# Kernel optimization log

Hardware: AMD Instinct MI355X
Metric: run time of the kernel (lower is better)

The kernel has to match this reference:

```python
import jax, jax.numpy as jnp
import numpy as np

B, S, E, H, R = 2, 1024, 1024, 16, 32
D = E // H  # head_dim = 64


def setup_inputs() -> dict:
    key = jax.random.key(0)
    ks = jax.random.split(key, 8)
    f = jax.random.normal
    return {
        "query": f(ks[0], (B, S, E), jnp.float32),
        "key": f(ks[1], (B, S, E), jnp.float32),  # unused by the module's forward, kept for signature fidelity
        "value": f(ks[2], (B, S, E), jnp.float32),
        "rules_keys": f(ks[3], (H, R, D), jnp.float32) * 0.02,   # nn.init.normal_(std=0.02)
        "rules_widths": jnp.ones((H, R, D), jnp.float32),
        "Wq": f(ks[4], (E, E), jnp.float32) * (E ** -0.5),
        "bq": jnp.zeros((E,), jnp.float32),
        "Wv": f(ks[5], (E * R, E), jnp.float32) * (E ** -0.5),
        "bv": jnp.zeros((E * R,), jnp.float32),
        "Wo": f(ks[6], (E, E), jnp.float32) * (E ** -0.5),
        "bo": jnp.zeros((E,), jnp.float32),
    }


def reference(query, key, value, rules_keys, rules_widths, Wq, bq, Wv, bv, Wo, bo):
    scale = D ** -0.5
    # query projection -> per-head layout (B,S,H,D)
    q = ((query @ Wq.T) + bq) * scale
    q = q.reshape(B, S, H, D)
    # fuzzy Gaussian membership: L1 distance to rule keys, scaled by widths,
    # HTSK -> mean over head_dim. z: (B,S,H,R)
    diff = jnp.abs(q[:, :, :, None, :] - rules_keys[None, None])        # (B,S,H,R,D)
    z = -0.5 * jnp.mean((diff / rules_widths[None, None]) ** 2, axis=-1)  # (B,S,H,R)
    attn = jax.nn.softmax(z, axis=-1)  # softmax over rules (dropout p=0 -> identity)
    # value projection to per-rule values: (B,S,H,R,D)
    v = ((value @ Wv.T) + bv) * scale
    v = v.reshape(B, S, H, D, R).transpose(0, 1, 2, 4, 3)
    # rule-weighted aggregation
    out = jnp.einsum('bshr,bshrd->bshd', attn, v)  # (B,S,H,D)
    # faithful to original torch code: transpose(1,2) then view(B,-1,H*D)
    # (this is a head-major flatten, reproduced exactly)
    out = out.transpose(0, 2, 1, 3).reshape(B, S, H * D)
    return (out @ Wo.T) + bo
```

## Files before the change

kernel.cpp:

```cpp
#include <hip/hip_runtime.h>
#include <hip/hip_bf16.h>
#include <cstdint>

typedef float f32x4 __attribute__((ext_vector_type(4)));
typedef short bf16x8 __attribute__((ext_vector_type(8)));

__device__ __forceinline__ unsigned short f32_to_bf16_rne(float f) {
  unsigned int u = __float_as_uint(f);
  return (unsigned short)((u + 0x7FFFu + ((u >> 16) & 1u)) >> 16);
}

#define GLOAD_LDS16(gptr, lptr)                                                             \
  __builtin_amdgcn_global_load_lds((const __attribute__((address_space(1))) unsigned int*)(gptr), \
                                   (__attribute__((address_space(3))) unsigned int*)(lptr), 16, 0, 0)

__global__ __launch_bounds__(256) void cvt_all(const float* __restrict__ wv,
                                               const float* __restrict__ q,
                                               const float* __restrict__ v,
                                               const float* __restrict__ wq,
                                               const float* __restrict__ wo,
                                               unsigned short* __restrict__ wvb,
                                               unsigned short* __restrict__ qb,
                                               unsigned short* __restrict__ vb,
                                               unsigned short* __restrict__ wqb,
                                               unsigned short* __restrict__ wob) {
  int i = blockIdx.x * 256 + threadIdx.x;
  const float* src;
  unsigned short* dst;
  int off;
  if (i < 4194304)      { src = wv; dst = wvb; off = i; }
  else if (i < 4456448) { src = q;  dst = qb;  off = i - 4194304; }
  else if (i < 4718592) { src = v;  dst = vb;  off = i - 4456448; }
  else if (i < 4849664) { src = wq; dst = wqb; off = i - 4718592; }
  else                  { src = wo; dst = wob; off = i - 4849664; }
  const float4* s = (const float4*)src;
  float4 a = s[2 * off], b = s[2 * off + 1];
  uint4 o;
  o.x = (unsigned)f32_to_bf16_rne(a.x) | ((unsigned)f32_to_bf16_rne(a.y) << 16);
  o.y = (unsigned)f32_to_bf16_rne(a.z) | ((unsigned)f32_to_bf16_rne(a.w) << 16);
  o.z = (unsigned)f32_to_bf16_rne(b.x) | ((unsigned)f32_to_bf16_rne(b.y) << 16);
  o.w = (unsigned)f32_to_bf16_rne(b.z) | ((unsigned)f32_to_bf16_rne(b.w) << 16);
  ((uint4*)dst)[off] = o;
}

__global__ __launch_bounds__(256) void fuzzy2_k(const float* __restrict__ qf,
                                                const float* __restrict__ rk,
                                                const float* __restrict__ rw,
                                                float* __restrict__ attn) {
  __shared__ float lk[32][65];
  __shared__ float lc[32][65];
  const int tid = threadIdx.x;
  const int h = blockIdx.y;
  const int mbase = blockIdx.x * 128;

  for (int idx = tid; idx < 2048; idx += 256) {
    int r = idx >> 6, d = idx & 63;
    lk[r][d] = rk[(size_t)(h * 32 + r) * 64 + d];
    float w = rw[(size_t)(h * 32 + r) * 64 + d];
    lc[r][d] = 0.0078125f / (w * w);
  }
  __syncthreads();

  const int g = tid >> 5;
  const int r = tid & 31;
#pragma unroll 1
  for (int it = 0; it < 16; ++it) {
    int m = mbase + it * 8 + g;
    const float* qrow = qf + (size_t)m * 1024 + h * 64;
    float acc = 0.f;
#pragma unroll
    for (int d0 = 0; d0 < 64; d0 += 4) {
      float4 q4 = *(const float4*)(qrow + d0);
      const float* qp = (const float*)&q4;
#pragma unroll
      for (int j = 0; j < 4; ++j) {
        float diff = qp[j] - lk[r][d0 + j];
        acc += lc[r][d0 + j] * diff * diff;
      }
    }
    float z = -acc;
    float mx = z;
#pragma unroll
    for (int mask = 16; mask >= 1; mask >>= 1) mx = fmaxf(mx, __shfl_xor(mx, mask));
    float e = __expf(z - mx);
    float s = e;
#pragma unroll
    for (int mask = 16; mask >= 1; mask >>= 1) s += __shfl_xor(s, mask);
    attn[(size_t)m * 512 + h * 32 + r] = e / s;
  }
}

__global__ __launch_bounds__(256) void gemm_bt64(const unsigned short* __restrict__ A,
                                                 const unsigned short* __restrict__ W,
                                                 const float* __restrict__ bias, float scale,
                                                 int M, int N, int K, float* __restrict__ Cf) {
  constexpr int BM = 64, BN = 128, BK = 32;
  __shared__ unsigned short As[2][BM * BK];
  __shared__ unsigned short Bs[2][BN * BK];
  const int tid = threadIdx.x;
  const int wid = tid >> 6;
  const int lane = tid & 63;
  const int l15 = lane & 15;
  const int l4 = lane >> 4;
  const int bm = blockIdx.y * BM;
  const int bn = blockIdx.x * BN;
  const int wc = wid * 32;

  f32x4 acc[4][2];
#pragma unroll
  for (int i = 0; i < 4; ++i)
#pragma unroll
    for (int j = 0; j < 2; ++j) acc[i][j] = (f32x4){0.f, 0.f, 0.f, 0.f};

  const int nk = K / BK;
  auto stage = [&](int buf, int kt) {
    {
      int c = tid;
      int row = c >> 2, ch = c & 3;
      int sch = ch ^ ((row >> 1) & 3);
      GLOAD_LDS16(A + (size_t)(bm + row) * K + kt * BK + sch * 8, &As[buf][c * 8]);
    }
#pragma unroll
    for (int i = 0; i < 2; ++i) {
      int c = i * 256 + tid;
      int row = c >> 2, ch = c & 3;
      int sch = ch ^ ((row >> 1) & 3);
      GLOAD_LDS16(W + (size_t)(bn + row) * K + kt * BK + sch * 8, &Bs[buf][c * 8]);
    }
  };

  stage(0, 0);
  __syncthreads();

  for (int kt = 0; kt < nk; ++kt) {
    const int cur = kt & 1;
    if (kt + 1 < nk) stage(cur ^ 1, kt + 1);
    bf16x8 a[4], b[2];
#pragma unroll
    for (int mi = 0; mi < 4; ++mi) {
      int rl = mi * 16 + l15;
      int ph = (rl * 64 + l4 * 16) ^ ((((unsigned)rl >> 1) & 3) << 4);
      a[mi] = *(const bf16x8*)((const char*)&As[cur][0] + ph);
    }
#pragma unroll
    for (int ni = 0; ni < 2; ++ni) {
      int rl = wc + ni * 16 + l15;
      int ph = (rl * 64 + l4 * 16) ^ ((((unsigned)rl >> 1) & 3) << 4);
      b[ni] = *(const bf16x8*)((const char*)&Bs[cur][0] + ph);
    }
#pragma unroll
    for (int mi = 0; mi < 4; ++mi)
#pragma unroll
      for (int ni = 0; ni < 2; ++ni)
        acc[mi][ni] = __builtin_amdgcn_mfma_f32_16x16x32_bf16(a[mi], b[ni], acc[mi][ni], 0, 0, 0);
    __syncthreads();
  }

#pragma unroll
  for (int mi = 0; mi < 4; ++mi) {
#pragma unroll
    for (int ni = 0; ni < 2; ++ni) {
      int gm = bm + mi * 16 + l4 * 4;
      int gn = bn + wc + ni * 16 + l15;
      float bval = bias[gn];
#pragma unroll
      for (int q = 0; q < 4; ++q)
        Cf[(size_t)(gm + q) * N + gn] = (acc[mi][ni][q] + bval) * scale;
    }
  }
}

__global__ __launch_bounds__(512) void gemm2_k(const unsigned short* __restrict__ A,
                                               const unsigned short* __restrict__ W,
                                               const float* __restrict__ bias, float scale,
                                               const float* __restrict__ attn,
                                               unsigned short* __restrict__ X) {
  constexpr int K = 1024, BK = 32, NK = K / BK;
  extern __shared__ unsigned short lds[];
  unsigned short* Asl = lds;
  unsigned short* Bsl = lds + 32768;
  const int tid = threadIdx.x;
  const int wid = tid >> 6, lane = tid & 63;
  const int l15 = lane & 15, l4 = lane >> 4;
  const int wm = wid >> 2, wn = wid & 3;

  int orig = blockIdx.x;
  int swz = (orig & 7) * 128 + (orig >> 3);
  const int bm = (swz & 7) * 256, bn = (swz >> 3) * 256;

  auto stageA = [&](int buf, int kt) {
#pragma unroll
    for (int i = 0; i < 2; ++i) {
      int c = i * 512 + tid;
      int row = c >> 2, ch = c & 3;
      int sch = ch ^ ((row >> 1) & 3);
      GLOAD_LDS16(A + (size_t)(bm + row) * K + kt * BK + sch * 8, Asl + buf * 8192 + c * 8);
    }
  };
  auto stageB = [&](int buf, int kt) {
#pragma unroll
    for (int i = 0; i < 2; ++i) {
      int c = i * 512 + tid;
      int row = c >> 2, ch = c & 3;
      int sch = ch ^ ((row >> 1) & 3);
      GLOAD_LDS16(W + (size_t)(bn + row) * K + kt * BK + sch * 8, Bsl + buf * 8192 + c * 8);
    }
  };

  f32x4 acc[8][4];
#pragma unroll
  for (int i = 0; i < 8; ++i)
#pragma unroll
    for (int j = 0; j < 4; ++j) acc[i][j] = (f32x4){0.f, 0.f, 0.f, 0.f};

  bf16x8 a0[8], a1[8], b[4];

#define FRAG_PH(rl) (((rl) * 64 + l4 * 16) ^ ((((unsigned)(rl) >> 1) & 3) << 4))

#define BODY(aC, aN, Tt, DO_STAGE, WN)                                                    \
  do {                                                                                    \
    if (DO_STAGE) {                                                                       \
      stageA(((Tt) + 2) & 3, (Tt) + 2);                                                   \
      stageB(((Tt) + 2) & 3, (Tt) + 2);                                                   \
    }                                                                                     \
    asm volatile("s_waitcnt vmcnt(" #WN ")" ::: "memory");                                \
    __builtin_amdgcn_s_barrier();                                                         \
    {                                                                                     \
      const char* _ab = (const char*)(Asl + (((Tt) + 1) & 3) * 8192);                     \
      const char* _bb = (const char*)(Bsl + (((Tt) + 1) & 3) * 8192);                     \
      __builtin_amdgcn_s_setprio(1);                                                      \
      _Pragma("unroll") for (int nf = 0; nf < 4; ++nf) {                                  \
        _Pragma("unroll") for (int mf = 0; mf < 8; ++mf)                                  \
          acc[mf][nf] =                                                                   \
              __builtin_amdgcn_mfma_f32_16x16x32_bf16(aC[mf], b[nf], acc[mf][nf], 0, 0, 0); \
        {                                                                                 \
          int rl = wn * 64 + nf * 16 + l15;                                               \
          b[nf] = *(const bf16x8*)(_bb + FRAG_PH(rl));                                    \
        }                                                                                 \
        _Pragma("unroll") for (int t = 0; t < 2; ++t) {                                   \
          int mf2 = nf * 2 + t;                                                           \
          int rl = wm * 128 + mf2 * 16 + l15;                                             \
          aN[mf2] = *(const bf16x8*)(_ab + FRAG_PH(rl));                                  \
        }                                                                                 \
      }                                                                                   \
      __builtin_amdgcn_s_setprio(0);                                                      \
    }                                                                                     \
    asm volatile("s_waitcnt lgkmcnt(0)" ::: "memory");                                    \
    __builtin_amdgcn_sched_barrier(0);                                                    \
  } while (0)

  stageA(0, 0); stageB(0, 0);
  stageA(1, 1); stageB(1, 1);
  asm volatile("s_waitcnt vmcnt(4)" ::: "memory");
  __builtin_amdgcn_s_barrier();
#pragma unroll
  for (int nf = 0; nf < 4; ++nf) {
    int rl = wn * 64 + nf * 16 + l15;
    b[nf] = *(const bf16x8*)((const char*)Bsl + FRAG_PH(rl));
  }
#pragma unroll
  for (int mf = 0; mf < 8; ++mf) {
    int rl = wm * 128 + mf * 16 + l15;
    a0[mf] = *(const bf16x8*)((const char*)Asl + FRAG_PH(rl));
  }
  asm volatile("s_waitcnt lgkmcnt(0)" ::: "memory");
  __builtin_amdgcn_sched_barrier(0);

  for (int T = 0; T < 30; T += 2) {
    BODY(a0, a1, T, 1, 4);
    BODY(a1, a0, (T + 1), 1, 4);
  }
  BODY(a0, a1, 30, 0, 0);
  __builtin_amdgcn_s_setprio(1);
#pragma unroll
  for (int nf = 0; nf < 4; ++nf)
#pragma unroll
    for (int mf = 0; mf < 8; ++mf)
      acc[mf][nf] = __builtin_amdgcn_mfma_f32_16x16x32_bf16(a1[mf], b[nf], acc[mf][nf], 0, 0, 0);
  __builtin_amdgcn_s_setprio(0);
#undef BODY
#undef FRAG_PH

  const int h = bn >> 11;
  const int dbase = ((bn & 2047) + wn * 64) >> 5;
#pragma unroll
  for (int mf = 0; mf < 8; ++mf) {
    int gm0 = bm + wm * 128 + mf * 16 + l4 * 4;
    float red[4][2];
#pragma unroll
    for (int q = 0; q < 4; ++q) { red[q][0] = 0.f; red[q][1] = 0.f; }
#pragma unroll
    for (int nf = 0; nf < 4; ++nf) {
      int col = bn + wn * 64 + nf * 16 + l15;
      float bval = bias[col];
      int r = (nf & 1) * 16 + l15;
      int g = nf >> 1;
#pragma unroll
      for (int q = 0; q < 4; ++q) {
        float w = attn[(size_t)(gm0 + q) * 512 + h * 32 + r];
        red[q][g] += (acc[mf][nf][q] + bval) * w;
      }
    }
#pragma unroll
    for (int q = 0; q < 4; ++q)
#pragma unroll
      for (int g = 0; g < 2; ++g) {
        float vv = red[q][g];
        for (int mask = 1; mask < 16; mask <<= 1) vv += __shfl_xor(vv, mask);
        red[q][g] = vv * scale;
      }
    if (l15 == 0) {
#pragma unroll
      for (int q = 0; q < 4; ++q) {
        int m = gm0 + q;
        int bb = m >> 10, s = m & 1023;
        size_t base = (((size_t)(bb * 16 + h)) * 1024 + s) * 64;
        unsigned lo = f32_to_bf16_rne(red[q][0]);
        unsigned hi = f32_to_bf16_rne(red[q][1]);
        ((unsigned*)X)[(base + dbase) >> 1] = lo | (hi << 16);
      }
    }
  }
}

extern "C" void kernel_launch(void* const* d_in, const int* in_sizes, int n_in, void* d_out,
                              int out_size, void* d_ws, size_t ws_size, hipStream_t stream) {
  const float* query = (const float*)d_in[0];
  const float* value = (const float*)d_in[2];
  const float* rk = (const float*)d_in[3];
  const float* rw = (const float*)d_in[4];
  const float* Wq = (const float*)d_in[5];
  const float* bq = (const float*)d_in[6];
  const float* Wv = (const float*)d_in[7];
  const float* bv = (const float*)d_in[8];
  const float* Wo = (const float*)d_in[9];
  const float* bo = (const float*)d_in[10];
  float* out = (float*)d_out;

  const float scale = 0.125f;

  char* p = (char*)d_ws;
  unsigned short* Wv_b = (unsigned short*)p; p += (size_t)33554432 * 2;
  unsigned short* Aq_b = (unsigned short*)p; p += (size_t)2097152 * 2;
  unsigned short* Av_b = (unsigned short*)p; p += (size_t)2097152 * 2;
  unsigned short* Wq_b = (unsigned short*)p; p += (size_t)1048576 * 2;
  unsigned short* Wo_b = (unsigned short*)p; p += (size_t)1048576 * 2;
  float* qf = (float*)p;   p += (size_t)2097152 * 4;
  float* attn = (float*)p; p += (size_t)1048576 * 4;
  unsigned short* X = (unsigned short*)p;

  cvt_all<<<19456, 256, 0, stream>>>(Wv, query, value, Wq, Wo, Wv_b, Aq_b, Av_b, Wq_b, Wo_b);

  gemm_bt64<<<dim3(8, 32), 256, 0, stream>>>(Aq_b, Wq_b, bq, scale, 2048, 1024, 1024, qf);
  fuzzy2_k<<<dim3(16, 16), 256, 0, stream>>>(qf, rk, rw, attn);
  hipFuncSetAttribute((const void*)gemm2_k, hipFuncAttributeMaxDynamicSharedMemorySize, 131072);
  gemm2_k<<<1024, 512, 131072, stream>>>(Av_b, Wv_b, bv, scale, attn, X);
  gemm_bt64<<<dim3(8, 32), 256, 0, stream>>>(X, Wo_b, bo, 1.0f, 2048, 1024, 1024, out);
}
```

Baseline: 238.5 us.

## Shrink GEMM tiles and switch big GEMM to triple-buffered 128x256 tiles

The small projection GEMMs move from 64x128 to 64x64 tiles with a 2x2 wave layout, doubling the grid. The big Wv GEMM moves from 256x256 to 128x256 tiles with a three-stage LDS ring (72 KB instead of 128 KB), a single A-fragment register set instead of double buffering, and launch bounds allowing more resident blocks. The aim is better occupancy and latency hiding, especially for the large fused GEMM. The cost is less data reuse per tile, so more global and LDS traffic per flop.

```diff
diff --git a/kernel.cpp b/kernel.cpp
--- a/kernel.cpp
+++ b/kernel.cpp
@@ -94,39 +94,32 @@
                                                  const unsigned short* __restrict__ W,
                                                  const float* __restrict__ bias, float scale,
                                                  int M, int N, int K, float* __restrict__ Cf) {
-  constexpr int BM = 64, BN = 128, BK = 32;
-  __shared__ unsigned short As[2][BM * BK];
-  __shared__ unsigned short Bs[2][BN * BK];
+  constexpr int BK = 32;
+  __shared__ unsigned short As[2][64 * BK];
+  __shared__ unsigned short Bs[2][64 * BK];
   const int tid = threadIdx.x;
   const int wid = tid >> 6;
   const int lane = tid & 63;
   const int l15 = lane & 15;
   const int l4 = lane >> 4;
-  const int bm = blockIdx.y * BM;
-  const int bn = blockIdx.x * BN;
-  const int wc = wid * 32;
-
-  f32x4 acc[4][2];
-#pragma unroll
-  for (int i = 0; i < 4; ++i)
+  const int bm = blockIdx.y * 64;
+  const int bn = blockIdx.x * 64;
+  const int wr = (wid >> 1) * 32;
+  const int wc = (wid & 1) * 32;
+
+  f32x4 acc[2][2];
+#pragma unroll
+  for (int i = 0; i < 2; ++i)
 #pragma unroll
     for (int j = 0; j < 2; ++j) acc[i][j] = (f32x4){0.f, 0.f, 0.f, 0.f};
 
   const int nk = K / BK;
   auto stage = [&](int buf, int kt) {
-    {
-      int c = tid;
-      int row = c >> 2, ch = c & 3;
-      int sch = ch ^ ((row >> 1) & 3);
-      GLOAD_LDS16(A + (size_t)(bm + row) * K + kt * BK + sch * 8, &As[buf][c * 8]);
-    }
-#pragma unroll
-    for (int i = 0; i < 2; ++i) {
-      int c = i * 256 + tid;
-      int row = c >> 2, ch = c & 3;
-      int sch = ch ^ ((row >> 1) & 3);
-      GLOAD_LDS16(W + (size_t)(bn + row) * K + kt * BK + sch * 8, &Bs[buf][c * 8]);
-    }
+    int c = tid;
+    int row = c >> 2, ch = c & 3;
+    int sch = ch ^ ((row >> 1) & 3);
+    GLOAD_LDS16(A + (size_t)(bm + row) * K + kt * BK + sch * 8, &As[buf][c * 8]);
+    GLOAD_LDS16(W + (size_t)(bn + row) * K + kt * BK + sch * 8, &Bs[buf][c * 8]);
   };
 
   stage(0, 0);
@@ -135,10 +128,10 @@
   for (int kt = 0; kt < nk; ++kt) {
     const int cur = kt & 1;
     if (kt + 1 < nk) stage(cur ^ 1, kt + 1);
-    bf16x8 a[4], b[2];
-#pragma unroll
-    for (int mi = 0; mi < 4; ++mi) {
-      int rl = mi * 16 + l15;
+    bf16x8 a[2], b[2];
+#pragma unroll
+    for (int mi = 0; mi < 2; ++mi) {
+      int rl = wr + mi * 16 + l15;
       int ph = (rl * 64 + l4 * 16) ^ ((((unsigned)rl >> 1) & 3) << 4);
       a[mi] = *(const bf16x8*)((const char*)&As[cur][0] + ph);
     }
@@ -149,7 +142,7 @@
       b[ni] = *(const bf16x8*)((const char*)&Bs[cur][0] + ph);
     }
 #pragma unroll
-    for (int mi = 0; mi < 4; ++mi)
+    for (int mi = 0; mi < 2; ++mi)
 #pragma unroll
       for (int ni = 0; ni < 2; ++ni)
         acc[mi][ni] = __builtin_amdgcn_mfma_f32_16x16x32_bf16(a[mi], b[ni], acc[mi][ni], 0, 0, 0);
@@ -157,10 +150,10 @@
   }
 
 #pragma unroll
-  for (int mi = 0; mi < 4; ++mi) {
+  for (int mi = 0; mi < 2; ++mi) {
 #pragma unroll
     for (int ni = 0; ni < 2; ++ni) {
-      int gm = bm + mi * 16 + l4 * 4;
+      int gm = bm + wr + mi * 16 + l4 * 4;
       int gn = bn + wc + ni * 16 + l15;
       float bval = bias[gn];
 #pragma unroll
@@ -170,32 +163,29 @@
   }
 }
 
-__global__ __launch_bounds__(512) void gemm2_k(const unsigned short* __restrict__ A,
-                                               const unsigned short* __restrict__ W,
-                                               const float* __restrict__ bias, float scale,
-                                               const float* __restrict__ attn,
-                                               unsigned short* __restrict__ X) {
+__global__ __launch_bounds__(512, 4) void gemm2_k(const unsigned short* __restrict__ A,
+                                                  const unsigned short* __restrict__ W,
+                                                  const float* __restrict__ bias, float scale,
+                                                  const float* __restrict__ attn,
+                                                  unsigned short* __restrict__ X) {
   constexpr int K = 1024, BK = 32, NK = K / BK;
   extern __shared__ unsigned short lds[];
   unsigned short* Asl = lds;
-  unsigned short* Bsl = lds + 32768;
+  unsigned short* Bsl = lds + 3 * 4096;
   const int tid = threadIdx.x;
   const int wid = tid >> 6, lane = tid & 63;
   const int l15 = lane & 15, l4 = lane >> 4;
   const int wm = wid >> 2, wn = wid & 3;
 
   int orig = blockIdx.x;
-  int swz = (orig & 7) * 128 + (orig >> 3);
-  const int bm = (swz & 7) * 256, bn = (swz >> 3) * 256;
+  int swz = (orig & 7) * 256 + (orig >> 3);
+  const int bm = (swz & 15) * 128, bn = (swz >> 4) * 256;
 
   auto stageA = [&](int buf, int kt) {
-#pragma unroll
-    for (int i = 0; i < 2; ++i) {
-      int c = i * 512 + tid;
-      int row = c >> 2, ch = c & 3;
-      int sch = ch ^ ((row >> 1) & 3);
-      GLOAD_LDS16(A + (size_t)(bm + row) * K + kt * BK + sch * 8, Asl + buf * 8192 + c * 8);
-    }
+    int c = tid;
+    int row = c >> 2, ch = c & 3;
+    int sch = ch ^ ((row >> 1) & 3);
+    GLOAD_LDS16(A + (size_t)(bm + row) * K + kt * BK + sch * 8, Asl + buf * 4096 + c * 8);
   };
   auto stageB = [&](int buf, int kt) {
 #pragma unroll
@@ -207,41 +197,36 @@
     }
   };
 
-  f32x4 acc[8][4];
-#pragma unroll
-  for (int i = 0; i < 8; ++i)
+  f32x4 acc[4][4];
+#pragma unroll
+  for (int i = 0; i < 4; ++i)
 #pragma unroll
     for (int j = 0; j < 4; ++j) acc[i][j] = (f32x4){0.f, 0.f, 0.f, 0.f};
 
-  bf16x8 a0[8], a1[8], b[4];
+  bf16x8 a[4], b[4];
 
 #define FRAG_PH(rl) (((rl) * 64 + l4 * 16) ^ ((((unsigned)(rl) >> 1) & 3) << 4))
 
-#define BODY(aC, aN, Tt, DO_STAGE, WN)                                                    \
+#define BODY(CUR, NXT, STG, Tt, DO_STAGE, WN)                                             \
   do {                                                                                    \
-    if (DO_STAGE) {                                                                       \
-      stageA(((Tt) + 2) & 3, (Tt) + 2);                                                   \
-      stageB(((Tt) + 2) & 3, (Tt) + 2);                                                   \
-    }                                                                                     \
+    if (DO_STAGE) { stageA(STG, (Tt) + 2); stageB(STG, (Tt) + 2); }                       \
     asm volatile("s_waitcnt vmcnt(" #WN ")" ::: "memory");                                \
     __builtin_amdgcn_s_barrier();                                                         \
     {                                                                                     \
-      const char* _ab = (const char*)(Asl + (((Tt) + 1) & 3) * 8192);                     \
-      const char* _bb = (const char*)(Bsl + (((Tt) + 1) & 3) * 8192);                     \
+      const char* _ab = (const char*)(Asl + (NXT) * 4096);                                \
+      const char* _bb = (const char*)(Bsl + (NXT) * 8192);                                \
       __builtin_amdgcn_s_setprio(1);                                                      \
-      _Pragma("unroll") for (int nf = 0; nf < 4; ++nf) {                                  \
-        _Pragma("unroll") for (int mf = 0; mf < 8; ++mf)                                  \
+      _Pragma("unroll") for (int mf = 0; mf < 4; ++mf) {                                  \
+        _Pragma("unroll") for (int nf = 0; nf < 4; ++nf) {                                \
           acc[mf][nf] =                                                                   \
-              __builtin_amdgcn_mfma_f32_16x16x32_bf16(aC[mf], b[nf], acc[mf][nf], 0, 0, 0); \
-        {                                                                                 \
-          int rl = wn * 64 + nf * 16 + l15;                                               \
-          b[nf] = *(const bf16x8*)(_bb + FRAG_PH(rl));                                    \
+              __builtin_amdgcn_mfma_f32_16x16x32_bf16(a[mf], b[nf], acc[mf][nf], 0, 0, 0);\
+          if (mf == 3) {                                                                  \
+            int rl = wn * 64 + nf * 16 + l15;                                             \
+            b[nf] = *(const bf16x8*)(_bb + FRAG_PH(rl));                                  \
+          }                                                                               \
         }                                                                                 \
-        _Pragma("unroll") for (int t = 0; t < 2; ++t) {                                   \
-          int mf2 = nf * 2 + t;                                                           \
-          int rl = wm * 128 + mf2 * 16 + l15;                                             \
-          aN[mf2] = *(const bf16x8*)(_ab + FRAG_PH(rl));                                  \
-        }                                                                                 \
+        int rl = wm * 64 + mf * 16 + l15;                                                 \
+        a[mf] = *(const bf16x8*)(_ab + FRAG_PH(rl));                                      \
       }                                                                                   \
       __builtin_amdgcn_s_setprio(0);                                                      \
     }                                                                                     \
@@ -251,7 +236,7 @@
 
   stageA(0, 0); stageB(0, 0);
   stageA(1, 1); stageB(1, 1);
-  asm volatile("s_waitcnt vmcnt(4)" ::: "memory");
+  asm volatile("s_waitcnt vmcnt(3)" ::: "memory");
   __builtin_amdgcn_s_barrier();
 #pragma unroll
   for (int nf = 0; nf < 4; ++nf) {
@@ -259,24 +244,25 @@
     b[nf] = *(const bf16x8*)((const char*)Bsl + FRAG_PH(rl));
   }
 #pragma unroll
-  for (int mf = 0; mf < 8; ++mf) {
-    int rl = wm * 128 + mf * 16 + l15;
-    a0[mf] = *(const bf16x8*)((const char*)Asl + FRAG_PH(rl));
+  for (int mf = 0; mf < 4; ++mf) {
+    int rl = wm * 64 + mf * 16 + l15;
+    a[mf] = *(const bf16x8*)((const char*)Asl + FRAG_PH(rl));
   }
   asm volatile("s_waitcnt lgkmcnt(0)" ::: "memory");
   __builtin_amdgcn_sched_barrier(0);
 
-  for (int T = 0; T < 30; T += 2) {
-    BODY(a0, a1, T, 1, 4);
-    BODY(a1, a0, (T + 1), 1, 4);
-  }
-  BODY(a0, a1, 30, 0, 0);
+  for (int T = 0; T < 30; T += 3) {
+    BODY(0, 1, 2, T, 1, 3);
+    BODY(1, 2, 0, (T + 1), 1, 3);
+    BODY(2, 0, 1, (T + 2), 1, 3);
+  }
+  BODY(0, 1, 2, 30, 0, 0);
   __builtin_amdgcn_s_setprio(1);
 #pragma unroll
-  for (int nf = 0; nf < 4; ++nf)
-#pragma unroll
-    for (int mf = 0; mf < 8; ++mf)
-      acc[mf][nf] = __builtin_amdgcn_mfma_f32_16x16x32_bf16(a1[mf], b[nf], acc[mf][nf], 0, 0, 0);
+  for (int mf = 0; mf < 4; ++mf)
+#pragma unroll
+    for (int nf = 0; nf < 4; ++nf)
+      acc[mf][nf] = __builtin_amdgcn_mfma_f32_16x16x32_bf16(a[mf], b[nf], acc[mf][nf], 0, 0, 0);
   __builtin_amdgcn_s_setprio(0);
 #undef BODY
 #undef FRAG_PH
@@ -284,8 +270,8 @@
   const int h = bn >> 11;
   const int dbase = ((bn & 2047) + wn * 64) >> 5;
 #pragma unroll
-  for (int mf = 0; mf < 8; ++mf) {
-    int gm0 = bm + wm * 128 + mf * 16 + l4 * 4;
+  for (int mf = 0; mf < 4; ++mf) {
+    int gm0 = bm + wm * 64 + mf * 16 + l4 * 4;
     float red[4][2];
 #pragma unroll
     for (int q = 0; q < 4; ++q) { red[q][0] = 0.f; red[q][1] = 0.f; }
@@ -351,9 +337,9 @@
 
   cvt_all<<<19456, 256, 0, stream>>>(Wv, query, value, Wq, Wo, Wv_b, Aq_b, Av_b, Wq_b, Wo_b);
 
-  gemm_bt64<<<dim3(8, 32), 256, 0, stream>>>(Aq_b, Wq_b, bq, scale, 2048, 1024, 1024, qf);
+  gemm_bt64<<<dim3(16, 32), 256, 0, stream>>>(Aq_b, Wq_b, bq, scale, 2048, 1024, 1024, qf);
   fuzzy2_k<<<dim3(16, 16), 256, 0, stream>>>(qf, rk, rw, attn);
-  hipFuncSetAttribute((const void*)gemm2_k, hipFuncAttributeMaxDynamicSharedMemorySize, 131072);
-  gemm2_k<<<1024, 512, 131072, stream>>>(Av_b, Wv_b, bv, scale, attn, X);
-  gemm_bt64<<<dim3(8, 32), 256, 0, stream>>>(X, Wo_b, bo, 1.0f, 2048, 1024, 1024, out);
-}
+  hipFuncSetAttribute((const void*)gemm2_k, hipFuncAttributeMaxDynamicSharedMemorySize, 73728);
+  gemm2_k<<<2048, 512, 73728, stream>>>(Av_b, Wv_b, bv, scale, attn, X);
+  gemm_bt64<<<dim3(16, 32), 256, 0, stream>>>(X, Wo_b, bo, 1.0f, 2048, 1024, 1024, out);
+}
```

Measured after the change: 235.2 us. No clear change (-1.4%).
